# Kernel tuning notes

Measured on AMD Instinct MI355X. Metric: run time of the kernel, lower is better.

The kernel has to match this reference:

```python
import jax, jax.numpy as jnp
import numpy as np

B, M, D = 8, 2048, 1024
F = 2048          # ffn_dim
N = 32            # num_experts
P = 4             # slots_per_expert


def setup_inputs() -> dict:
    key = jax.random.key(0)
    ks = jax.random.split(key, 6)
    # kaiming-uniform-ish bounds
    bp = 1.0 / np.sqrt(D)
    b1w = 1.0 / np.sqrt(D)
    b2w = 1.0 / np.sqrt(F)
    return {
        "x": jax.random.normal(ks[0], (B, M, D), dtype=jnp.float32),
        "phi": jax.random.uniform(ks[1], (D, N, P), jnp.float32, -bp, bp),
        "w1": jax.random.uniform(ks[2], (N, D, F), jnp.float32, -b1w, b1w),
        "b1": jax.random.uniform(ks[3], (N, F), jnp.float32, -b1w, b1w),
        "w2": jax.random.uniform(ks[4], (N, F, D), jnp.float32, -b2w, b2w),
        "b2": jax.random.uniform(ks[5], (N, D), jnp.float32, -b2w, b2w),
    }


def reference(x, phi, w1, b1, w2, b2):
    # logits: (b, m, n, p)
    logits = jnp.einsum("bmd,dnp->bmnp", x, phi)
    # dispatch: softmax over sequence dim m
    dispatch = jax.nn.softmax(logits, axis=1)
    # combine: softmax over flattened (n*p) slot dim
    b, m, n, p = logits.shape
    combine = jax.nn.softmax(logits.reshape(b, m, n * p), axis=-1).reshape(b, m, n, p)
    # dispatch tokens to slots: (b, n, p, d)
    xs = jnp.einsum("bmd,bmnp->bnpd", x, dispatch)
    # expert layer 1 + ReLU^2
    h = jnp.einsum("bnpd,ndf->bnpf", xs, w1) + b1[None, :, None, :]
    h = jnp.square(jax.nn.relu(h))
    # expert layer 2
    y = jnp.einsum("bnpf,nfd->bnpd", h, w2) + b2[None, :, None, :]
    # combine slot outputs back to tokens: (b, m, d)
    return jnp.einsum("bnpd,bmnp->bmd", y, combine)
```

## Files before the change

kernel.cpp:

```cpp
#include <hip/hip_runtime.h>

#define BB   8
#define MM   2048
#define DD   1024
#define FF   2048
#define NE   32
#define PP   4
#define NPS  128
#define BMR  16384

__global__ __launch_bounds__(256) void k1_logits_kernel(
    const float* __restrict__ x, const float* __restrict__ phi,
    float* __restrict__ Ebuf, float* __restrict__ Cbuf, float* __restrict__ colsum)
{
    __shared__ __align__(16) float a_lds[32][36];
    __shared__ __align__(16) float b_lds[32][128];
    const int tid  = threadIdx.x;
    const int row0 = blockIdx.x * 32;
    const int bidx = row0 >> 11;
    const int c4 = tid & 31, r4 = tid >> 5;
    const int c0 = c4 * 4,   r0 = r4 * 4;
    const int kk = tid & 31, rr0 = tid >> 5;

    float acc[4][4] = {};
    for (int kt = 0; kt < 32; ++kt) {
        const int k0 = kt * 32;
        #pragma unroll
        for (int i = 0; i < 4; ++i) {
            const int rr = rr0 + 8 * i;
            a_lds[kk][rr] = x[(size_t)(row0 + rr) * DD + k0 + kk];
        }
        #pragma unroll
        for (int i = 0; i < 4; ++i) {
            const int idx = tid + 256 * i;
            const int bkk = idx >> 5, bc = (idx & 31) * 4;
            *(float4*)&b_lds[bkk][bc] = *(const float4*)&phi[(size_t)(k0 + bkk) * NPS + bc];
        }
        __syncthreads();
        #pragma unroll
        for (int k = 0; k < 32; ++k) {
            const float4 av4 = *(const float4*)&a_lds[k][r0];
            const float4 bv4 = *(const float4*)&b_lds[k][c0];
            const float ar[4] = {av4.x, av4.y, av4.z, av4.w};
            const float br[4] = {bv4.x, bv4.y, bv4.z, bv4.w};
            #pragma unroll
            for (int i = 0; i < 4; ++i)
                #pragma unroll
                for (int j = 0; j < 4; ++j)
                    acc[i][j] = fmaf(ar[i], br[j], acc[i][j]);
        }
        __syncthreads();
    }

    float e[4][4];
    #pragma unroll
    for (int i = 0; i < 4; ++i)
        #pragma unroll
        for (int j = 0; j < 4; ++j)
            e[i][j] = __expf(acc[i][j]);

    #pragma unroll
    for (int i = 0; i < 4; ++i) {
        float4 v = make_float4(e[i][0], e[i][1], e[i][2], e[i][3]);
        *(float4*)&Ebuf[(size_t)(row0 + r0 + i) * NPS + c0] = v;
    }

    #pragma unroll
    for (int i = 0; i < 4; ++i)
        a_lds[r0 + i][c4] = e[i][0] + e[i][1] + e[i][2] + e[i][3];
    __syncthreads();
    float inv[4];
    #pragma unroll
    for (int i = 0; i < 4; ++i) {
        float s = 0.f;
        for (int c = 0; c < 32; ++c) s += a_lds[r0 + i][c];
        inv[i] = 1.0f / s;
    }
    #pragma unroll
    for (int i = 0; i < 4; ++i) {
        float4 v = make_float4(e[i][0] * inv[i], e[i][1] * inv[i],
                               e[i][2] * inv[i], e[i][3] * inv[i]);
        *(float4*)&Cbuf[(size_t)(row0 + r0 + i) * NPS + c0] = v;
    }

    float* bred = &b_lds[0][0];
    #pragma unroll
    for (int j = 0; j < 4; ++j)
        bred[(c0 + j) * 8 + r4] = e[0][j] + e[1][j] + e[2][j] + e[3][j];
    __syncthreads();
    if (tid < NPS) {
        float s = 0.f;
        #pragma unroll
        for (int g = 0; g < 8; ++g) s += bred[tid * 8 + g];
        atomicAdd(&colsum[bidx * NPS + tid], s);
    }
}

__global__ __launch_bounds__(256) void k2_xs_kernel(
    const float* __restrict__ Ebuf, const float* __restrict__ x,
    const float* __restrict__ colsum, float* __restrict__ xs)
{
    __shared__ __align__(16) float a_lds[32][34];
    __shared__ __align__(16) float b_lds[32][64];
    const int tid = threadIdx.x;
    const int bx  = blockIdx.x;
    const int bidx = bx >> 6;
    const int rem  = bx & 63;
    const int np0  = (rem >> 4) * 32;
    const int d0   = (rem & 15) * 64;
    const int cg = tid & 15, rg = tid >> 4;
    const int kk = tid & 31, rr0 = tid >> 5;

    float acc[2][4] = {};
    for (int kt = 0; kt < 64; ++kt) {
        const int m0 = kt * 32;
        #pragma unroll
        for (int i = 0; i < 4; ++i) {
            const int mm = rr0 + 8 * i;
            a_lds[mm][kk] = Ebuf[((size_t)bidx * MM + m0 + mm) * NPS + np0 + kk];
        }
        #pragma unroll
        for (int i = 0; i < 2; ++i) {
            const int idx = tid + 256 * i;
            const int mm = idx >> 4, cc = (idx & 15) * 4;
            *(float4*)&b_lds[mm][cc] =
                *(const float4*)&x[((size_t)bidx * MM + m0 + mm) * DD + d0 + cc];
        }
        __syncthreads();
        #pragma unroll
        for (int k = 0; k < 32; ++k) {
            const float2 av2 = *(const float2*)&a_lds[k][rg * 2];
            const float4 bv4 = *(const float4*)&b_lds[k][cg * 4];
            const float ar[2] = {av2.x, av2.y};
            const float br[4] = {bv4.x, bv4.y, bv4.z, bv4.w};
            #pragma unroll
            for (int i = 0; i < 2; ++i)
                #pragma unroll
                for (int j = 0; j < 4; ++j)
                    acc[i][j] = fmaf(ar[i], br[j], acc[i][j]);
        }
        __syncthreads();
    }
    #pragma unroll
    for (int i = 0; i < 2; ++i) {
        const int np = np0 + rg * 2 + i;
        const float inv = 1.0f / colsum[bidx * NPS + np];
        float4 v = make_float4(acc[i][0] * inv, acc[i][1] * inv,
                               acc[i][2] * inv, acc[i][3] * inv);
        *(float4*)&xs[((size_t)bidx * NPS + np) * DD + d0 + cg * 4] = v;
    }
}

__global__ __launch_bounds__(256) void k3_ffn1_kernel(
    const float* __restrict__ xs, const float* __restrict__ w1,
    const float* __restrict__ b1, float* __restrict__ h)
{
    __shared__ __align__(16) float a_lds[32][36];
    __shared__ __align__(16) float b_lds[32][128];
    const int tid = threadIdx.x;
    const int n  = blockIdx.x >> 4;
    const int f0 = (blockIdx.x & 15) * 128;
    const int c4 = tid & 31, r4 = tid >> 5;
    const int c0 = c4 * 4,   r0 = r4 * 4;
    const int kk = tid & 31, rr0 = tid >> 5;

    size_t a_base[4];
    #pragma unroll
    for (int i = 0; i < 4; ++i) {
        const int rr = rr0 + 8 * i;
        const int bi = rr >> 2, p = rr & 3;
        a_base[i] = ((size_t)bi * NPS + n * PP + p) * DD + kk;
    }
    const size_t w_row = (size_t)n * DD;

    float  a_reg[4];
    float4 b_reg[4];
    #pragma unroll
    for (int i = 0; i < 4; ++i) a_reg[i] = xs[a_base[i]];
    #pragma unroll
    for (int i = 0; i < 4; ++i) {
        const int idx = tid + 256 * i;
        const int bkk = idx >> 5, bc = (idx & 31) * 4;
        b_reg[i] = *(const float4*)&w1[(w_row + bkk) * FF + f0 + bc];
    }

    float acc[4][4] = {};
    for (int kt = 0; kt < 32; ++kt) {
        #pragma unroll
        for (int i = 0; i < 4; ++i) a_lds[kk][rr0 + 8 * i] = a_reg[i];
        #pragma unroll
        for (int i = 0; i < 4; ++i) {
            const int idx = tid + 256 * i;
            *(float4*)&b_lds[idx >> 5][(idx & 31) * 4] = b_reg[i];
        }
        __syncthreads();
        if (kt < 31) {
            const int k0 = (kt + 1) * 32;
            #pragma unroll
            for (int i = 0; i < 4; ++i) a_reg[i] = xs[a_base[i] + k0];
            #pragma unroll
            for (int i = 0; i < 4; ++i) {
                const int idx = tid + 256 * i;
                const int bkk = idx >> 5, bc = (idx & 31) * 4;
                b_reg[i] = *(const float4*)&w1[(w_row + k0 + bkk) * FF + f0 + bc];
            }
        }
        #pragma unroll
        for (int k = 0; k < 32; ++k) {
            const float4 av4 = *(const float4*)&a_lds[k][r0];
            const float4 bv4 = *(const float4*)&b_lds[k][c0];
            const float ar[4] = {av4.x, av4.y, av4.z, av4.w};
            const float br[4] = {bv4.x, bv4.y, bv4.z, bv4.w};
            #pragma unroll
            for (int i = 0; i < 4; ++i)
                #pragma unroll
                for (int j = 0; j < 4; ++j)
                    acc[i][j] = fmaf(ar[i], br[j], acc[i][j]);
        }
        __syncthreads();
    }

    const float4 b1v = *(const float4*)&b1[n * FF + f0 + c0];
    const float bb1[4] = {b1v.x, b1v.y, b1v.z, b1v.w};
    #pragma unroll
    for (int i = 0; i < 4; ++i) {
        const int rr = r0 + i;
        const int bi = rr >> 2, p = rr & 3;
        float v[4];
        #pragma unroll
        for (int j = 0; j < 4; ++j) {
            float t = fmaxf(acc[i][j] + bb1[j], 0.0f);
            v[j] = t * t;
        }
        *(float4*)&h[((size_t)bi * NPS + n * PP + p) * FF + f0 + c0] =
            make_float4(v[0], v[1], v[2], v[3]);
    }
}

__global__ __launch_bounds__(256) void k4_ffn2_kernel(
    const float* __restrict__ h, const float* __restrict__ w2,
    const float* __restrict__ b2, float* __restrict__ y)
{
    __shared__ __align__(16) float a_lds[32][34];
    __shared__ __align__(16) float b_lds[32][64];
    const int tid = threadIdx.x;
    const int n  = blockIdx.x >> 4;
    const int d0 = (blockIdx.x & 15) * 64;
    const int cg = tid & 15, rg = tid >> 4;
    const int kk = tid & 31, rr0 = tid >> 5;

    size_t a_base[4];
    #pragma unroll
    for (int i = 0; i < 4; ++i) {
        const int rr = rr0 + 8 * i;
        const int bi = rr >> 2, p = rr & 3;
        a_base[i] = ((size_t)bi * NPS + n * PP + p) * FF + kk;
    }
    const size_t w_base = (size_t)n * FF;

    float  a_reg[4];
    float4 b_reg[2];
    #pragma unroll
    for (int i = 0; i < 4; ++i) a_reg[i] = h[a_base[i]];
    #pragma unroll
    for (int i = 0; i < 2; ++i) {
        const int idx = tid + 256 * i;
        const int bkk = idx >> 4, cc = (idx & 15) * 4;
        b_reg[i] = *(const float4*)&w2[(w_base + bkk) * DD + d0 + cc];
    }

    float acc[2][4] = {};
    for (int kt = 0; kt < 64; ++kt) {
        #pragma unroll
        for (int i = 0; i < 4; ++i) a_lds[kk][rr0 + 8 * i] = a_reg[i];
        #pragma unroll
        for (int i = 0; i < 2; ++i) {
            const int idx = tid + 256 * i;
            *(float4*)&b_lds[idx >> 4][(idx & 15) * 4] = b_reg[i];
        }
        __syncthreads();
        if (kt < 63) {
            const int k0 = (kt + 1) * 32;
            #pragma unroll
            for (int i = 0; i < 4; ++i) a_reg[i] = h[a_base[i] + k0];
            #pragma unroll
            for (int i = 0; i < 2; ++i) {
                const int idx = tid + 256 * i;
                const int bkk = idx >> 4, cc = (idx & 15) * 4;
                b_reg[i] = *(const float4*)&w2[(w_base + k0 + bkk) * DD + d0 + cc];
            }
        }
        #pragma unroll
        for (int k = 0; k < 32; ++k) {
            const float2 av2 = *(const float2*)&a_lds[k][rg * 2];
            const float4 bv4 = *(const float4*)&b_lds[k][cg * 4];
            const float ar[2] = {av2.x, av2.y};
            const float br[4] = {bv4.x, bv4.y, bv4.z, bv4.w};
            #pragma unroll
            for (int i = 0; i < 2; ++i)
                #pragma unroll
                for (int j = 0; j < 4; ++j)
                    acc[i][j] = fmaf(ar[i], br[j], acc[i][j]);
        }
        __syncthreads();
    }

    const float4 b2v = *(const float4*)&b2[n * DD + d0 + cg * 4];
    #pragma unroll
    for (int i = 0; i < 2; ++i) {
        const int rr = rg * 2 + i;
        const int bi = rr >> 2, p = rr & 3;
        float4 v = make_float4(acc[i][0] + b2v.x, acc[i][1] + b2v.y,
                               acc[i][2] + b2v.z, acc[i][3] + b2v.w);
        *(float4*)&y[((size_t)bi * NPS + n * PP + p) * DD + d0 + cg * 4] = v;
    }
}

__global__ __launch_bounds__(256) void k5_out_kernel(
    const float* __restrict__ Cbuf, const float* __restrict__ y,
    float* __restrict__ out)
{
    __shared__ __align__(16) float a_lds[32][36];
    __shared__ __align__(16) float b_lds[32][128];
    const int tid = threadIdx.x;
    const int bx  = blockIdx.x;
    const int bidx = bx >> 9;
    const int rem  = bx & 511;
    const int m0 = (rem >> 3) * 32;
    const int d0 = (rem & 7) * 128;
    const int c4 = tid & 31, r4 = tid >> 5;
    const int c0 = c4 * 4,   r0 = r4 * 4;
    const int kk = tid & 31, rr0 = tid >> 5;

    float acc[4][4] = {};
    for (int kt = 0; kt < 4; ++kt) {
        const int k0 = kt * 32;
        #pragma unroll
        for (int i = 0; i < 4; ++i) {
            const int rr = rr0 + 8 * i;
            a_lds[kk][rr] = Cbuf[((size_t)bidx * MM + m0 + rr) * NPS + k0 + kk];
        }
        #pragma unroll
        for (int i = 0; i < 4; ++i) {
            const int idx = tid + 256 * i;
            const int bkk = idx >> 5, bc = (idx & 31) * 4;
            *(float4*)&b_lds[bkk][bc] =
                *(const float4*)&y[((size_t)bidx * NPS + k0 + bkk) * DD + d0 + bc];
        }
        __syncthreads();
        #pragma unroll
        for (int k = 0; k < 32; ++k) {
            const float4 av4 = *(const float4*)&a_lds[k][r0];
            const float4 bv4 = *(const float4*)&b_lds[k][c0];
            const float ar[4] = {av4.x, av4.y, av4.z, av4.w};
            const float br[4] = {bv4.x, bv4.y, bv4.z, bv4.w};
            #pragma unroll
            for (int i = 0; i < 4; ++i)
                #pragma unroll
                for (int j = 0; j < 4; ++j)
                    acc[i][j] = fmaf(ar[i], br[j], acc[i][j]);
        }
        __syncthreads();
    }
    #pragma unroll
    for (int i = 0; i < 4; ++i) {
        float4 v = make_float4(acc[i][0], acc[i][1], acc[i][2], acc[i][3]);
        *(float4*)&out[((size_t)bidx * MM + m0 + r0 + i) * DD + d0 + c0] = v;
    }
}

extern "C" void kernel_launch(void* const* d_in, const int* in_sizes, int n_in,
                              void* d_out, int out_size, void* d_ws, size_t ws_size,
                              hipStream_t stream)
{
    const float* x   = (const float*)d_in[0];
    const float* phi = (const float*)d_in[1];
    const float* w1  = (const float*)d_in[2];
    const float* b1  = (const float*)d_in[3];
    const float* w2  = (const float*)d_in[4];
    const float* b2  = (const float*)d_in[5];
    float* out = (float*)d_out;
    float* ws  = (float*)d_ws;

    float* Ebuf   = ws;
    float* Cbuf   = Ebuf  + 2097152;
    float* xsbuf  = Cbuf  + 2097152;
    float* hbuf   = xsbuf + 1048576;
    float* ybuf   = hbuf  + 2097152;
    float* colsum = ybuf  + 1048576;

    hipMemsetAsync(colsum, 0, BB * NPS * sizeof(float), stream);
    hipLaunchKernelGGL(k1_logits_kernel, dim3(512), dim3(256), 0, stream,
                       x, phi, Ebuf, Cbuf, colsum);
    hipLaunchKernelGGL(k2_xs_kernel, dim3(512), dim3(256), 0, stream,
                       Ebuf, x, colsum, xsbuf);
    hipLaunchKernelGGL(k3_ffn1_kernel, dim3(512), dim3(256), 0, stream,
                       xsbuf, w1, b1, hbuf);
    hipLaunchKernelGGL(k4_ffn2_kernel, dim3(512), dim3(256), 0, stream,
                       hbuf, w2, b2, ybuf);
    hipLaunchKernelGGL(k5_out_kernel, dim3(4096), dim3(256), 0, stream,
                       Cbuf, ybuf, out);
}
```

Before: 851.6 us.

## Enlarge GEMM tiles, double-buffer LDS, split-K the dispatch GEMM with reduce pass

Logits and output-combine kernels move to 64x128 tiles with a 4x8 per-thread micro-tile, and the dispatch GEMM over the sequence is split into four K-chunks written to partial buffers, then summed by a new reduce kernel. Most kernels now use double-buffered shared memory with register prefetch, which removes the trailing barrier per K step. The FFN2 kernel's tile is widened to 128 columns. The aim is more arithmetic reuse per shared-memory load and more parallelism for the long-K dispatch GEMM, at the cost of an extra kernel launch, extra partial-buffer traffic and higher register pressure.

```diff
diff --git a/kernel.cpp b/kernel.cpp
--- a/kernel.cpp
+++ b/kernel.cpp
@@ -13,306 +13,371 @@
     const float* __restrict__ x, const float* __restrict__ phi,
     float* __restrict__ Ebuf, float* __restrict__ Cbuf, float* __restrict__ colsum)
 {
-    __shared__ __align__(16) float a_lds[32][36];
-    __shared__ __align__(16) float b_lds[32][128];
+    __shared__ __align__(16) float aA[2][32][68];
+    __shared__ __align__(16) float bB[2][32][128];
     const int tid  = threadIdx.x;
-    const int row0 = blockIdx.x * 32;
+    const int row0 = blockIdx.x * 64;
     const int bidx = row0 >> 11;
-    const int c4 = tid & 31, r4 = tid >> 5;
-    const int c0 = c4 * 4,   r0 = r4 * 4;
+    const int r0 = (tid >> 4) * 4;
+    const int c0 = (tid & 15) * 4;
+    const int sa_r = tid >> 2;
+    const int sa_k = (tid & 3) * 8;
+    const float* xa = x + (size_t)(row0 + sa_r) * DD + sa_k;
+
+    float4 ar0 = *(const float4*)(xa);
+    float4 ar1 = *(const float4*)(xa + 4);
+    float4 br[4];
+    #pragma unroll
+    for (int i = 0; i < 4; ++i) {
+        const int idx = tid + 256 * i;
+        br[i] = *(const float4*)&phi[(size_t)(idx >> 5) * NPS + (idx & 31) * 4];
+    }
+
+    float acc[4][8] = {};
+    for (int kt = 0; kt < 32; ++kt) {
+        const int buf = kt & 1;
+        {
+            const float a8[8] = {ar0.x,ar0.y,ar0.z,ar0.w, ar1.x,ar1.y,ar1.z,ar1.w};
+            #pragma unroll
+            for (int j = 0; j < 8; ++j) aA[buf][sa_k + j][sa_r] = a8[j];
+            #pragma unroll
+            for (int i = 0; i < 4; ++i) {
+                const int idx = tid + 256 * i;
+                *(float4*)&bB[buf][idx >> 5][(idx & 31) * 4] = br[i];
+            }
+        }
+        __syncthreads();
+        if (kt < 31) {
+            const int k0 = (kt + 1) * 32;
+            ar0 = *(const float4*)(xa + k0);
+            ar1 = *(const float4*)(xa + k0 + 4);
+            #pragma unroll
+            for (int i = 0; i < 4; ++i) {
+                const int idx = tid + 256 * i;
+                br[i] = *(const float4*)&phi[(size_t)(k0 + (idx >> 5)) * NPS + (idx & 31) * 4];
+            }
+        }
+        #pragma unroll
+        for (int k = 0; k < 32; ++k) {
+            const float4 av = *(const float4*)&aA[buf][k][r0];
+            const float4 b0 = *(const float4*)&bB[buf][k][c0];
+            const float4 b1 = *(const float4*)&bB[buf][k][64 + c0];
+            const float arr[4] = {av.x, av.y, av.z, av.w};
+            const float brr[8] = {b0.x,b0.y,b0.z,b0.w, b1.x,b1.y,b1.z,b1.w};
+            #pragma unroll
+            for (int i = 0; i < 4; ++i)
+                #pragma unroll
+                for (int j = 0; j < 8; ++j)
+                    acc[i][j] = fmaf(arr[i], brr[j], acc[i][j]);
+        }
+    }
+
+    #pragma unroll
+    for (int i = 0; i < 4; ++i)
+        #pragma unroll
+        for (int j = 0; j < 8; ++j)
+            acc[i][j] = __expf(acc[i][j]);
+
+    #pragma unroll
+    for (int i = 0; i < 4; ++i) {
+        const size_t rb = (size_t)(row0 + r0 + i) * NPS;
+        *(float4*)&Ebuf[rb + c0]      = make_float4(acc[i][0], acc[i][1], acc[i][2], acc[i][3]);
+        *(float4*)&Ebuf[rb + 64 + c0] = make_float4(acc[i][4], acc[i][5], acc[i][6], acc[i][7]);
+    }
+
+    float* red = (float*)aA;
+    #pragma unroll
+    for (int i = 0; i < 4; ++i) {
+        float s = 0.f;
+        #pragma unroll
+        for (int j = 0; j < 8; ++j) s += acc[i][j];
+        red[(r0 + i) * 16 + (tid & 15)] = s;
+    }
+    __syncthreads();
+    #pragma unroll
+    for (int i = 0; i < 4; ++i) {
+        float s = 0.f;
+        #pragma unroll
+        for (int t = 0; t < 16; ++t) s += red[(r0 + i) * 16 + t];
+        const float inv = 1.0f / s;
+        const size_t rb = (size_t)(row0 + r0 + i) * NPS;
+        *(float4*)&Cbuf[rb + c0]      = make_float4(acc[i][0]*inv, acc[i][1]*inv,
+                                                    acc[i][2]*inv, acc[i][3]*inv);
+        *(float4*)&Cbuf[rb + 64 + c0] = make_float4(acc[i][4]*inv, acc[i][5]*inv,
+                                                    acc[i][6]*inv, acc[i][7]*inv);
+    }
+
+    float* cred = (float*)bB;
+    const int g = tid >> 4;
+    #pragma unroll
+    for (int j = 0; j < 8; ++j) {
+        const int col = (j < 4) ? (c0 + j) : (64 + c0 + j - 4);
+        cred[col * 16 + g] = acc[0][j] + acc[1][j] + acc[2][j] + acc[3][j];
+    }
+    __syncthreads();
+    if (tid < NPS) {
+        float s = 0.f;
+        #pragma unroll
+        for (int t = 0; t < 16; ++t) s += cred[tid * 16 + t];
+        atomicAdd(&colsum[bidx * NPS + tid], s);
+    }
+}
+
+__global__ __launch_bounds__(256) void k2_xs_kernel(
+    const float* __restrict__ Ebuf, const float* __restrict__ x,
+    const float* __restrict__ colsum, float* __restrict__ xsp)
+{
+    __shared__ __align__(16) float aA[2][32][68];
+    __shared__ __align__(16) float bB[2][32][128];
+    const int tid = threadIdx.x;
+    const int bx  = blockIdx.x;
+    const int ks  = bx & 3;
+    const int dt  = (bx >> 2) & 7;
+    const int npt = (bx >> 5) & 1;
+    const int b   = bx >> 6;
+    const int np0 = npt * 64;
+    const int d0  = dt * 128;
+    const size_t mb = (size_t)b * MM + ks * 512;
+    const int r0 = (tid >> 4) * 4;
+    const int c0 = (tid & 15) * 4;
+
+    float4 ea[2], br[4];
+    #pragma unroll
+    for (int i = 0; i < 2; ++i) {
+        const int idx = tid + 256 * i;
+        ea[i] = *(const float4*)&Ebuf[(mb + (idx >> 4)) * NPS + np0 + (idx & 15) * 4];
+    }
+    #pragma unroll
+    for (int i = 0; i < 4; ++i) {
+        const int idx = tid + 256 * i;
+        br[i] = *(const float4*)&x[(mb + (idx >> 5)) * DD + d0 + (idx & 31) * 4];
+    }
+
+    float acc[4][8] = {};
+    for (int kt = 0; kt < 16; ++kt) {
+        const int buf = kt & 1;
+        #pragma unroll
+        for (int i = 0; i < 2; ++i) {
+            const int idx = tid + 256 * i;
+            const int am = idx >> 4, ac = (idx & 15) * 4;
+            aA[buf][am][ac + 0] = ea[i].x;
+            aA[buf][am][ac + 1] = ea[i].y;
+            aA[buf][am][ac + 2] = ea[i].z;
+            aA[buf][am][ac + 3] = ea[i].w;
+        }
+        #pragma unroll
+        for (int i = 0; i < 4; ++i) {
+            const int idx = tid + 256 * i;
+            *(float4*)&bB[buf][idx >> 5][(idx & 31) * 4] = br[i];
+        }
+        __syncthreads();
+        if (kt < 15) {
+            const int k0 = (kt + 1) * 32;
+            #pragma unroll
+            for (int i = 0; i < 2; ++i) {
+                const int idx = tid + 256 * i;
+                ea[i] = *(const float4*)&Ebuf[(mb + k0 + (idx >> 4)) * NPS + np0 + (idx & 15) * 4];
+            }
+            #pragma unroll
+            for (int i = 0; i < 4; ++i) {
+                const int idx = tid + 256 * i;
+                br[i] = *(const float4*)&x[(mb + k0 + (idx >> 5)) * DD + d0 + (idx & 31) * 4];
+            }
+        }
+        #pragma unroll
+        for (int k = 0; k < 32; ++k) {
+            const float4 av = *(const float4*)&aA[buf][k][r0];
+            const float4 b0 = *(const float4*)&bB[buf][k][c0];
+            const float4 b1 = *(const float4*)&bB[buf][k][64 + c0];
+            const float arr[4] = {av.x, av.y, av.z, av.w};
+            const float brr[8] = {b0.x,b0.y,b0.z,b0.w, b1.x,b1.y,b1.z,b1.w};
+            #pragma unroll
+            for (int i = 0; i < 4; ++i)
+                #pragma unroll
+                for (int j = 0; j < 8; ++j)
+                    acc[i][j] = fmaf(arr[i], brr[j], acc[i][j]);
+        }
+    }
+
+    #pragma unroll
+    for (int i = 0; i < 4; ++i) {
+        const int np = np0 + r0 + i;
+        const float inv = 1.0f / colsum[b * NPS + np];
+        const size_t ob = ((size_t)(ks * BB + b) * NPS + np) * DD + d0;
+        *(float4*)&xsp[ob + c0]      = make_float4(acc[i][0]*inv, acc[i][1]*inv,
+                                                   acc[i][2]*inv, acc[i][3]*inv);
+        *(float4*)&xsp[ob + 64 + c0] = make_float4(acc[i][4]*inv, acc[i][5]*inv,
+                                                   acc[i][6]*inv, acc[i][7]*inv);
+    }
+}
+
+__global__ __launch_bounds__(256) void k2b_reduce_kernel(
+    const float* __restrict__ xsp, float* __restrict__ xs)
+{
+    const size_t i = ((size_t)blockIdx.x * 256 + threadIdx.x) * 4;
+    const float4 a = *(const float4*)&xsp[i];
+    const float4 b = *(const float4*)&xsp[i + 1048576];
+    const float4 c = *(const float4*)&xsp[i + 2097152];
+    const float4 d = *(const float4*)&xsp[i + 3145728];
+    *(float4*)&xs[i] = make_float4(a.x+b.x+c.x+d.x, a.y+b.y+c.y+d.y,
+                                   a.z+b.z+c.z+d.z, a.w+b.w+c.w+d.w);
+}
+
+__global__ __launch_bounds__(256) void k3_ffn1_kernel(
+    const float* __restrict__ xs, const float* __restrict__ w1,
+    const float* __restrict__ b1, float* __restrict__ h)
+{
+    __shared__ __align__(16) float aA[2][32][36];
+    __shared__ __align__(16) float bB[2][32][128];
+    const int tid = threadIdx.x;
+    const int n  = blockIdx.x >> 4;
+    const int f0 = (blockIdx.x & 15) * 128;
+    const int r0 = (tid >> 5) * 4;
+    const int c0 = (tid & 31) * 4;
     const int kk = tid & 31, rr0 = tid >> 5;
+
+    size_t a_base[4];
+    #pragma unroll
+    for (int i = 0; i < 4; ++i) {
+        const int rr = rr0 + 8 * i;
+        a_base[i] = ((size_t)(rr >> 2) * NPS + n * PP + (rr & 3)) * DD + kk;
+    }
+    const size_t wrow = (size_t)n * DD;
+
+    float  a_reg[4];
+    float4 b_reg[4];
+    #pragma unroll
+    for (int i = 0; i < 4; ++i) a_reg[i] = xs[a_base[i]];
+    #pragma unroll
+    for (int i = 0; i < 4; ++i) {
+        const int idx = tid + 256 * i;
+        b_reg[i] = *(const float4*)&w1[(wrow + (idx >> 5)) * FF + f0 + (idx & 31) * 4];
+    }
 
     float acc[4][4] = {};
     for (int kt = 0; kt < 32; ++kt) {
-        const int k0 = kt * 32;
-        #pragma unroll
-        for (int i = 0; i < 4; ++i) {
-            const int rr = rr0 + 8 * i;
-            a_lds[kk][rr] = x[(size_t)(row0 + rr) * DD + k0 + kk];
-        }
+        const int buf = kt & 1;
+        #pragma unroll
+        for (int i = 0; i < 4; ++i) aA[buf][kk][rr0 + 8 * i] = a_reg[i];
         #pragma unroll
         for (int i = 0; i < 4; ++i) {
             const int idx = tid + 256 * i;
-            const int bkk = idx >> 5, bc = (idx & 31) * 4;
-            *(float4*)&b_lds[bkk][bc] = *(const float4*)&phi[(size_t)(k0 + bkk) * NPS + bc];
-        }
-        __syncthreads();
+            *(float4*)&bB[buf][idx >> 5][(idx & 31) * 4] = b_reg[i];
+        }
+        __syncthreads();
+        if (kt < 31) {
+            const int k0 = (kt + 1) * 32;
+            #pragma unroll
+            for (int i = 0; i < 4; ++i) a_reg[i] = xs[a_base[i] + k0];
+            #pragma unroll
+            for (int i = 0; i < 4; ++i) {
+                const int idx = tid + 256 * i;
+                b_reg[i] = *(const float4*)&w1[(wrow + k0 + (idx >> 5)) * FF + f0 + (idx & 31) * 4];
+            }
+        }
         #pragma unroll
         for (int k = 0; k < 32; ++k) {
-            const float4 av4 = *(const float4*)&a_lds[k][r0];
-            const float4 bv4 = *(const float4*)&b_lds[k][c0];
-            const float ar[4] = {av4.x, av4.y, av4.z, av4.w};
-            const float br[4] = {bv4.x, bv4.y, bv4.z, bv4.w};
+            const float4 av = *(const float4*)&aA[buf][k][r0];
+            const float4 bv = *(const float4*)&bB[buf][k][c0];
+            const float arr[4] = {av.x, av.y, av.z, av.w};
+            const float brr[4] = {bv.x, bv.y, bv.z, bv.w};
             #pragma unroll
             for (int i = 0; i < 4; ++i)
                 #pragma unroll
                 for (int j = 0; j < 4; ++j)
-                    acc[i][j] = fmaf(ar[i], br[j], acc[i][j]);
-        }
-        __syncthreads();
-    }
-
-    float e[4][4];
-    #pragma unroll
-    for (int i = 0; i < 4; ++i)
-        #pragma unroll
-        for (int j = 0; j < 4; ++j)
-            e[i][j] = __expf(acc[i][j]);
-
-    #pragma unroll
-    for (int i = 0; i < 4; ++i) {
-        float4 v = make_float4(e[i][0], e[i][1], e[i][2], e[i][3]);
-        *(float4*)&Ebuf[(size_t)(row0 + r0 + i) * NPS + c0] = v;
-    }
-
-    #pragma unroll
-    for (int i = 0; i < 4; ++i)
-        a_lds[r0 + i][c4] = e[i][0] + e[i][1] + e[i][2] + e[i][3];
-    __syncthreads();
-    float inv[4];
-    #pragma unroll
-    for (int i = 0; i < 4; ++i) {
-        float s = 0.f;
-        for (int c = 0; c < 32; ++c) s += a_lds[r0 + i][c];
-        inv[i] = 1.0f / s;
-    }
-    #pragma unroll
-    for (int i = 0; i < 4; ++i) {
-        float4 v = make_float4(e[i][0] * inv[i], e[i][1] * inv[i],
-                               e[i][2] * inv[i], e[i][3] * inv[i]);
-        *(float4*)&Cbuf[(size_t)(row0 + r0 + i) * NPS + c0] = v;
-    }
-
-    float* bred = &b_lds[0][0];
-    #pragma unroll
-    for (int j = 0; j < 4; ++j)
-        bred[(c0 + j) * 8 + r4] = e[0][j] + e[1][j] + e[2][j] + e[3][j];
-    __syncthreads();
-    if (tid < NPS) {
-        float s = 0.f;
-        #pragma unroll
-        for (int g = 0; g < 8; ++g) s += bred[tid * 8 + g];
-        atomicAdd(&colsum[bidx * NPS + tid], s);
-    }
-}
-
-__global__ __launch_bounds__(256) void k2_xs_kernel(
-    const float* __restrict__ Ebuf, const float* __restrict__ x,
-    const float* __restrict__ colsum, float* __restrict__ xs)
-{
-    __shared__ __align__(16) float a_lds[32][34];
-    __shared__ __align__(16) float b_lds[32][64];
+                    acc[i][j] = fmaf(arr[i], brr[j], acc[i][j]);
+        }
+    }
+
+    const float4 b1v = *(const float4*)&b1[n * FF + f0 + c0];
+    const float bb1[4] = {b1v.x, b1v.y, b1v.z, b1v.w};
+    #pragma unroll
+    for (int i = 0; i < 4; ++i) {
+        const int rr = r0 + i;
+        float v[4];
+        #pragma unroll
+        for (int j = 0; j < 4; ++j) {
+            const float t = fmaxf(acc[i][j] + bb1[j], 0.0f);
+            v[j] = t * t;
+        }
+        *(float4*)&h[((size_t)(rr >> 2) * NPS + n * PP + (rr & 3)) * FF + f0 + c0] =
+            make_float4(v[0], v[1], v[2], v[3]);
+    }
+}
+
+__global__ __launch_bounds__(256) void k4_ffn2_kernel(
+    const float* __restrict__ h, const float* __restrict__ w2,
+    const float* __restrict__ b2, float* __restrict__ y)
+{
+    __shared__ __align__(16) float aA[2][32][36];
+    __shared__ __align__(16) float bB[2][32][128];
     const int tid = threadIdx.x;
-    const int bx  = blockIdx.x;
-    const int bidx = bx >> 6;
-    const int rem  = bx & 63;
-    const int np0  = (rem >> 4) * 32;
-    const int d0   = (rem & 15) * 64;
-    const int cg = tid & 15, rg = tid >> 4;
+    const int n  = blockIdx.x >> 3;
+    const int d0 = (blockIdx.x & 7) * 128;
+    const int r0 = (tid >> 5) * 4;
+    const int c0 = (tid & 31) * 4;
     const int kk = tid & 31, rr0 = tid >> 5;
 
-    float acc[2][4] = {};
-    for (int kt = 0; kt < 64; ++kt) {
-        const int m0 = kt * 32;
-        #pragma unroll
-        for (int i = 0; i < 4; ++i) {
-            const int mm = rr0 + 8 * i;
-            a_lds[mm][kk] = Ebuf[((size_t)bidx * MM + m0 + mm) * NPS + np0 + kk];
-        }
-        #pragma unroll
-        for (int i = 0; i < 2; ++i) {
-            const int idx = tid + 256 * i;
-            const int mm = idx >> 4, cc = (idx & 15) * 4;
-            *(float4*)&b_lds[mm][cc] =
-                *(const float4*)&x[((size_t)bidx * MM + m0 + mm) * DD + d0 + cc];
-        }
-        __syncthreads();
-        #pragma unroll
-        for (int k = 0; k < 32; ++k) {
-            const float2 av2 = *(const float2*)&a_lds[k][rg * 2];
-            const float4 bv4 = *(const float4*)&b_lds[k][cg * 4];
-            const float ar[2] = {av2.x, av2.y};
-            const float br[4] = {bv4.x, bv4.y, bv4.z, bv4.w};
-            #pragma unroll
-            for (int i = 0; i < 2; ++i)
-                #pragma unroll
-                for (int j = 0; j < 4; ++j)
-                    acc[i][j] = fmaf(ar[i], br[j], acc[i][j]);
-        }
-        __syncthreads();
-    }
-    #pragma unroll
-    for (int i = 0; i < 2; ++i) {
-        const int np = np0 + rg * 2 + i;
-        const float inv = 1.0f / colsum[bidx * NPS + np];
-        float4 v = make_float4(acc[i][0] * inv, acc[i][1] * inv,
-                               acc[i][2] * inv, acc[i][3] * inv);
-        *(float4*)&xs[((size_t)bidx * NPS + np) * DD + d0 + cg * 4] = v;
-    }
-}
-
-__global__ __launch_bounds__(256) void k3_ffn1_kernel(
-    const float* __restrict__ xs, const float* __restrict__ w1,
-    const float* __restrict__ b1, float* __restrict__ h)
-{
-    __shared__ __align__(16) float a_lds[32][36];
-    __shared__ __align__(16) float b_lds[32][128];
-    const int tid = threadIdx.x;
-    const int n  = blockIdx.x >> 4;
-    const int f0 = (blockIdx.x & 15) * 128;
-    const int c4 = tid & 31, r4 = tid >> 5;
-    const int c0 = c4 * 4,   r0 = r4 * 4;
-    const int kk = tid & 31, rr0 = tid >> 5;
-
     size_t a_base[4];
     #pragma unroll
     for (int i = 0; i < 4; ++i) {
         const int rr = rr0 + 8 * i;
-        const int bi = rr >> 2, p = rr & 3;
-        a_base[i] = ((size_t)bi * NPS + n * PP + p) * DD + kk;
-    }
-    const size_t w_row = (size_t)n * DD;
+        a_base[i] = ((size_t)(rr >> 2) * NPS + n * PP + (rr & 3)) * FF + kk;
+    }
+    const size_t wb = (size_t)n * FF;
 
     float  a_reg[4];
     float4 b_reg[4];
     #pragma unroll
-    for (int i = 0; i < 4; ++i) a_reg[i] = xs[a_base[i]];
-    #pragma unroll
-    for (int i = 0; i < 4; ++i) {
-        const int idx = tid + 256 * i;
-        const int bkk = idx >> 5, bc = (idx & 31) * 4;
-        b_reg[i] = *(const float4*)&w1[(w_row + bkk) * FF + f0 + bc];
+    for (int i = 0; i < 4; ++i) a_reg[i] = h[a_base[i]];
+    #pragma unroll
+    for (int i = 0; i < 4; ++i) {
+        const int idx = tid + 256 * i;
+        b_reg[i] = *(const float4*)&w2[(wb + (idx >> 5)) * DD + d0 + (idx & 31) * 4];
     }
 
     float acc[4][4] = {};
-    for (int kt = 0; kt < 32; ++kt) {
-        #pragma unroll
-        for (int i = 0; i < 4; ++i) a_lds[kk][rr0 + 8 * i] = a_reg[i];
+    for (int kt = 0; kt < 64; ++kt) {
+        const int buf = kt & 1;
+        #pragma unroll
+        for (int i = 0; i < 4; ++i) aA[buf][kk][rr0 + 8 * i] = a_reg[i];
         #pragma unroll
         for (int i = 0; i < 4; ++i) {
             const int idx = tid + 256 * i;
-            *(float4*)&b_lds[idx >> 5][(idx & 31) * 4] = b_reg[i];
-        }
-        __syncthreads();
-        if (kt < 31) {
+            *(float4*)&bB[buf][idx >> 5][(idx & 31) * 4] = b_reg[i];
+        }
+        __syncthreads();
+        if (kt < 63) {
             const int k0 = (kt + 1) * 32;
             #pragma unroll
-            for (int i = 0; i < 4; ++i) a_reg[i] = xs[a_base[i] + k0];
-            #pragma unroll
-            for (int i = 0; i < 4; ++i) {
-                const int idx = tid + 256 * i;
-                const int bkk = idx >> 5, bc = (idx & 31) * 4;
-                b_reg[i] = *(const float4*)&w1[(w_row + k0 + bkk) * FF + f0 + bc];
+            for (int i = 0; i < 4; ++i) a_reg[i] = h[a_base[i] + k0];
+            #pragma unroll
+            for (int i = 0; i < 4; ++i) {
+                const int idx = tid + 256 * i;
+                b_reg[i] = *(const float4*)&w2[(wb + k0 + (idx >> 5)) * DD + d0 + (idx & 31) * 4];
             }
         }
         #pragma unroll
         for (int k = 0; k < 32; ++k) {
-            const float4 av4 = *(const float4*)&a_lds[k][r0];
-            const float4 bv4 = *(const float4*)&b_lds[k][c0];
-            const float ar[4] = {av4.x, av4.y, av4.z, av4.w};
-            const float br[4] = {bv4.x, bv4.y, bv4.z, bv4.w};
+            const float4 av = *(const float4*)&aA[buf][k][r0];
+            const float4 bv = *(const float4*)&bB[buf][k][c0];
+            const float arr[4] = {av.x, av.y, av.z, av.w};
+            const float brr[4] = {bv.x, bv.y, bv.z, bv.w};
             #pragma unroll
             for (int i = 0; i < 4; ++i)
                 #pragma unroll
                 for (int j = 0; j < 4; ++j)
-                    acc[i][j] = fmaf(ar[i], br[j], acc[i][j]);
-        }
-        __syncthreads();
-    }
-
-    const float4 b1v = *(const float4*)&b1[n * FF + f0 + c0];
-    const float bb1[4] = {b1v.x, b1v.y, b1v.z, b1v.w};
+                    acc[i][j] = fmaf(arr[i], brr[j], acc[i][j]);
+        }
+    }
+
+    const float4 b2v = *(const float4*)&b2[n * DD + d0 + c0];
     #pragma unroll
     for (int i = 0; i < 4; ++i) {
         const int rr = r0 + i;
-        const int bi = rr >> 2, p = rr & 3;
-        float v[4];
-        #pragma unroll
-        for (int j = 0; j < 4; ++j) {
-            float t = fmaxf(acc[i][j] + bb1[j], 0.0f);
-            v[j] = t * t;
-        }
-        *(float4*)&h[((size_t)bi * NPS + n * PP + p) * FF + f0 + c0] =
-            make_float4(v[0], v[1], v[2], v[3]);
-    }
-}
-
-__global__ __launch_bounds__(256) void k4_ffn2_kernel(
-    const float* __restrict__ h, const float* __restrict__ w2,
-    const float* __restrict__ b2, float* __restrict__ y)
-{
-    __shared__ __align__(16) float a_lds[32][34];
-    __shared__ __align__(16) float b_lds[32][64];
-    const int tid = threadIdx.x;
-    const int n  = blockIdx.x >> 4;
-    const int d0 = (blockIdx.x & 15) * 64;
-    const int cg = tid & 15, rg = tid >> 4;
-    const int kk = tid & 31, rr0 = tid >> 5;
-
-    size_t a_base[4];
-    #pragma unroll
-    for (int i = 0; i < 4; ++i) {
-        const int rr = rr0 + 8 * i;
-        const int bi = rr >> 2, p = rr & 3;
-        a_base[i] = ((size_t)bi * NPS + n * PP + p) * FF + kk;
-    }
-    const size_t w_base = (size_t)n * FF;
-
-    float  a_reg[4];
-    float4 b_reg[2];
-    #pragma unroll
-    for (int i = 0; i < 4; ++i) a_reg[i] = h[a_base[i]];
-    #pragma unroll
-    for (int i = 0; i < 2; ++i) {
-        const int idx = tid + 256 * i;
-        const int bkk = idx >> 4, cc = (idx & 15) * 4;
-        b_reg[i] = *(const float4*)&w2[(w_base + bkk) * DD + d0 + cc];
-    }
-
-    float acc[2][4] = {};
-    for (int kt = 0; kt < 64; ++kt) {
-        #pragma unroll
-        for (int i = 0; i < 4; ++i) a_lds[kk][rr0 + 8 * i] = a_reg[i];
-        #pragma unroll
-        for (int i = 0; i < 2; ++i) {
-            const int idx = tid + 256 * i;
-            *(float4*)&b_lds[idx >> 4][(idx & 15) * 4] = b_reg[i];
-        }
-        __syncthreads();
-        if (kt < 63) {
-            const int k0 = (kt + 1) * 32;
-            #pragma unroll
-            for (int i = 0; i < 4; ++i) a_reg[i] = h[a_base[i] + k0];
-            #pragma unroll
-            for (int i = 0; i < 2; ++i) {
-                const int idx = tid + 256 * i;
-                const int bkk = idx >> 4, cc = (idx & 15) * 4;
-                b_reg[i] = *(const float4*)&w2[(w_base + k0 + bkk) * DD + d0 + cc];
-            }
-        }
-        #pragma unroll
-        for (int k = 0; k < 32; ++k) {
-            const float2 av2 = *(const float2*)&a_lds[k][rg * 2];
-            const float4 bv4 = *(const float4*)&b_lds[k][cg * 4];
-            const float ar[2] = {av2.x, av2.y};
-            const float br[4] = {bv4.x, bv4.y, bv4.z, bv4.w};
-            #pragma unroll
-            for (int i = 0; i < 2; ++i)
-                #pragma unroll
-                for (int j = 0; j < 4; ++j)
-                    acc[i][j] = fmaf(ar[i], br[j], acc[i][j]);
-        }
-        __syncthreads();
-    }
-
-    const float4 b2v = *(const float4*)&b2[n * DD + d0 + cg * 4];
-    #pragma unroll
-    for (int i = 0; i < 2; ++i) {
-        const int rr = rg * 2 + i;
-        const int bi = rr >> 2, p = rr & 3;
-        float4 v = make_float4(acc[i][0] + b2v.x, acc[i][1] + b2v.y,
-                               acc[i][2] + b2v.z, acc[i][3] + b2v.w);
-        *(float4*)&y[((size_t)bi * NPS + n * PP + p) * DD + d0 + cg * 4] = v;
+        const float4 v = make_float4(acc[i][0] + b2v.x, acc[i][1] + b2v.y,
+                                     acc[i][2] + b2v.z, acc[i][3] + b2v.w);
+        *(float4*)&y[((size_t)(rr >> 2) * NPS + n * PP + (rr & 3)) * DD + d0 + c0] = v;
     }
 }
 
@@ -320,52 +385,75 @@
     const float* __restrict__ Cbuf, const float* __restrict__ y,
     float* __restrict__ out)
 {
-    __shared__ __align__(16) float a_lds[32][36];
-    __shared__ __align__(16) float b_lds[32][128];
+    __shared__ __align__(16) float aA[32][68];
+    __shared__ __align__(16) float bB[32][128];
     const int tid = threadIdx.x;
     const int bx  = blockIdx.x;
-    const int bidx = bx >> 9;
-    const int rem  = bx & 511;
-    const int m0 = (rem >> 3) * 32;
-    const int d0 = (rem & 7) * 128;
-    const int c4 = tid & 31, r4 = tid >> 5;
-    const int c0 = c4 * 4,   r0 = r4 * 4;
-    const int kk = tid & 31, rr0 = tid >> 5;
-
-    float acc[4][4] = {};
+    const int dt = bx & 7;
+    const int mt = (bx >> 3) & 31;
+    const int b  = bx >> 8;
+    const int d0 = dt * 128;
+    const int m0 = mt * 64;
+    const int r0 = (tid >> 4) * 4;
+    const int c0 = (tid & 15) * 4;
+    const int sa_r = tid >> 2;
+    const int sa_k = (tid & 3) * 8;
+    const float* ca = Cbuf + ((size_t)b * MM + m0 + sa_r) * NPS + sa_k;
+    const size_t yb = (size_t)b * NPS;
+
+    float4 ar0 = *(const float4*)(ca);
+    float4 ar1 = *(const float4*)(ca + 4);
+    float4 br[4];
+    #pragma unroll
+    for (int i = 0; i < 4; ++i) {
+        const int idx = tid + 256 * i;
+        br[i] = *(const float4*)&y[(yb + (idx >> 5)) * DD + d0 + (idx & 31) * 4];
+    }
+
+    float acc[4][8] = {};
     for (int kt = 0; kt < 4; ++kt) {
-        const int k0 = kt * 32;
-        #pragma unroll
-        for (int i = 0; i < 4; ++i) {
-            const int rr = rr0 + 8 * i;
-            a_lds[kk][rr] = Cbuf[((size_t)bidx * MM + m0 + rr) * NPS + k0 + kk];
-        }
-        #pragma unroll
-        for (int i = 0; i < 4; ++i) {
-            const int idx = tid + 256 * i;
-            const int bkk = idx >> 5, bc = (idx & 31) * 4;
-            *(float4*)&b_lds[bkk][bc] =
-                *(const float4*)&y[((size_t)bidx * NPS + k0 + bkk) * DD + d0 + bc];
-        }
-        __syncthreads();
+        {
+            const float a8[8] = {ar0.x,ar0.y,ar0.z,ar0.w, ar1.x,ar1.y,ar1.z,ar1.w};
+            #pragma unroll
+            for (int j = 0; j < 8; ++j) aA[sa_k + j][sa_r] = a8[j];
+            #pragma unroll
+            for (int i = 0; i < 4; ++i) {
+                const int idx = tid + 256 * i;
+                *(float4*)&bB[idx >> 5][(idx & 31) * 4] = br[i];
+            }
+        }
+        __syncthreads();
+        if (kt < 3) {
+            const int k0 = (kt + 1) * 32;
+            ar0 = *(const float4*)(ca + k0);
+            ar1 = *(const float4*)(ca + k0 + 4);
+            #pragma unroll
+            for (int i = 0; i < 4; ++i) {
+                const int idx = tid + 256 * i;
+                br[i] = *(const float4*)&y[(yb + k0 + (idx >> 5)) * DD + d0 + (idx & 31) * 4];
+            }
+        }
         #pragma unroll
         for (int k = 0; k < 32; ++k) {
-            const float4 av4 = *(const float4*)&a_lds[k][r0];
-            const float4 bv4 = *(const float4*)&b_lds[k][c0];
-            const float ar[4] = {av4.x, av4.y, av4.z, av4.w};
-            const float br[4] = {bv4.x, bv4.y, bv4.z, bv4.w};
+            const float4 av = *(const float4*)&aA[k][r0];
+            const float4 b0 = *(const float4*)&bB[k][c0];
+            const float4 b1 = *(const float4*)&bB[k][64 + c0];
+            const float arr[4] = {av.x, av.y, av.z, av.w};
+            const float brr[8] = {b0.x,b0.y,b0.z,b0.w, b1.x,b1.y,b1.z,b1.w};
             #pragma unroll
             for (int i = 0; i < 4; ++i)
                 #pragma unroll
-                for (int j = 0; j < 4; ++j)
-                    acc[i][j] = fmaf(ar[i], br[j], acc[i][j]);
-        }
-        __syncthreads();
-    }
-    #pragma unroll
-    for (int i = 0; i < 4; ++i) {
-        float4 v = make_float4(acc[i][0], acc[i][1], acc[i][2], acc[i][3]);
-        *(float4*)&out[((size_t)bidx * MM + m0 + r0 + i) * DD + d0 + c0] = v;
+                for (int j = 0; j < 8; ++j)
+                    acc[i][j] = fmaf(arr[i], brr[j], acc[i][j]);
+        }
+        __syncthreads();
+    }
+
+    #pragma unroll
+    for (int i = 0; i < 4; ++i) {
+        const size_t ob = ((size_t)b * MM + m0 + r0 + i) * DD + d0;
+        *(float4*)&out[ob + c0]      = make_float4(acc[i][0], acc[i][1], acc[i][2], acc[i][3]);
+        *(float4*)&out[ob + 64 + c0] = make_float4(acc[i][4], acc[i][5], acc[i][6], acc[i][7]);
     }
 }
 
@@ -384,20 +472,23 @@
 
     float* Ebuf   = ws;
     float* Cbuf   = Ebuf  + 2097152;
-    float* xsbuf  = Cbuf  + 2097152;
+    float* xsp    = Cbuf  + 2097152;
+    float* xsbuf  = xsp   + 4194304;
     float* hbuf   = xsbuf + 1048576;
     float* ybuf   = hbuf  + 2097152;
     float* colsum = ybuf  + 1048576;
 
     hipMemsetAsync(colsum, 0, BB * NPS * sizeof(float), stream);
-    hipLaunchKernelGGL(k1_logits_kernel, dim3(512), dim3(256), 0, stream,
+    hipLaunchKernelGGL(k1_logits_kernel, dim3(256), dim3(256), 0, stream,
                        x, phi, Ebuf, Cbuf, colsum);
     hipLaunchKernelGGL(k2_xs_kernel, dim3(512), dim3(256), 0, stream,
-                       Ebuf, x, colsum, xsbuf);
+                       Ebuf, x, colsum, xsp);
+    hipLaunchKernelGGL(k2b_reduce_kernel, dim3(1024), dim3(256), 0, stream,
+                       xsp, xsbuf);
     hipLaunchKernelGGL(k3_ffn1_kernel, dim3(512), dim3(256), 0, stream,
                        xsbuf, w1, b1, hbuf);
-    hipLaunchKernelGGL(k4_ffn2_kernel, dim3(512), dim3(256), 0, stream,
+    hipLaunchKernelGGL(k4_ffn2_kernel, dim3(256), dim3(256), 0, stream,
                        hbuf, w2, b2, ybuf);
-    hipLaunchKernelGGL(k5_out_kernel, dim3(4096), dim3(256), 0, stream,
+    hipLaunchKernelGGL(k5_out_kernel, dim3(2048), dim3(256), 0, stream,
                        Cbuf, ybuf, out);
 }
```

Measured after the change: 896.3 us. 5.3% more time.
